# Performance work log

Hardware: AMD Instinct MI355X
Metric: run time of the kernel (lower is better)

Reference implementation:

```python
import jax, jax.numpy as jnp
import numpy as np

B, S, H = 2, 1024, 768
E, K, I = 16, 4, 768
ALPHA, LIMIT, EPS = 1.702, 7.0, 1e-5


def setup_inputs() -> dict:
    key = jax.random.key(0)
    ks = jax.random.split(key, 7)
    x = jax.random.normal(ks[0], (B, S, H), dtype=jnp.float32)
    scale = jnp.ones((H,), jnp.float32)                      # RMSNorm scale
    gate_w = jax.random.normal(ks[1], (E, H), jnp.float32) * 0.02
    gate_b = jnp.zeros((E,), jnp.float32)
    w1 = jax.random.normal(ks[2], (E, H, 2 * I), jnp.float32) * 0.02
    b1 = jax.random.normal(ks[3], (E, 2 * I), jnp.float32) * 0.02
    w2 = jax.random.normal(ks[4], (E, I, H), jnp.float32) * 0.02
    b2 = jax.random.normal(ks[5], (E, H), jnp.float32) * 0.02
    return {"x": x, "scale": scale, "gate_w": gate_w, "gate_b": gate_b,
            "w1": w1, "b1": b1, "w2": w2, "b2": b2}


def _swiglu(h):
    # chunk (not packed) split of last dim
    x_glu, x_lin = jnp.split(h, 2, axis=-1)
    x_glu = jnp.minimum(x_glu, LIMIT)
    x_lin = jnp.clip(x_lin, -LIMIT, LIMIT)
    return x_glu * jax.nn.sigmoid(ALPHA * x_glu) * (x_lin + 1.0)


def reference(x, scale, gate_w, gate_b, w1, b1, w2, b2):
    Bx, Sx, Hx = x.shape
    # RMSNorm in fp32 with learned scale
    xf = x.astype(jnp.float32)
    t = xf * jax.lax.rsqrt(jnp.mean(xf * xf, axis=-1, keepdims=True) + EPS) * scale
    t = t.reshape(-1, Hx)                                    # [T, H]
    T = t.shape[0]
    # Router: fp32 gate, top-k, softmax over selected logits, /K (re-scaled by K at combine)
    g = t @ gate_w.T + gate_b                                # [T, E]
    vals, idx = jax.lax.top_k(g, K)                          # [T, K]
    w = jax.nn.softmax(vals, axis=-1) / K                    # [T, K]
    # Scatter routing weights to dense [T, E]; unselected experts get weight 0,
    # so the dense per-expert compute below matches the gathered bmm path exactly.
    full_w = jnp.zeros((T, E), jnp.float32).at[jnp.arange(T)[:, None], idx].set(w)
    # Expert MLP1 + SwiGLU
    h = jnp.einsum('th,ehf->tef', t, w1) + b1                # [T, E, 2I]
    h = _swiglu(h)                                           # [T, E, I]
    # Expert MLP2
    y = jnp.einsum('tei,eih->teh', h, w2) + b2               # [T, E, H]
    # Weighted combine (einsum('bec,be->bc')) * experts_per_token
    out = jnp.einsum('teh,te->th', y, full_w) * K            # [T, H]
    # Residual connection
    return x + out.astype(x.dtype).reshape(Bx, Sx, Hx)
```

## Files before the change

### kernel.cpp

```cpp
#include <hip/hip_runtime.h>
#include <hip/hip_bf16.h>
#include <cstddef>

#define T_TOK 2048
#define H_DIM 768
#define NEXP 16
#define KSEL 4
#define I_DIM 768
#define TWO_I 1536
#define NSLOT (T_TOK*KSEL)
#define ALPHA 1.702f
#define LIMIT 7.0f
#define EPS_RMS 1e-5f
#define BM 128

typedef _Float16 f16;
typedef _Float16 half8 __attribute__((ext_vector_type(8)));
typedef float f32x4 __attribute__((ext_vector_type(4)));

__global__ __launch_bounds__(256) void k_rms_router(
    const float* __restrict__ x, const float* __restrict__ scale,
    const float* __restrict__ gw, const float* __restrict__ gb,
    f16* __restrict__ th, float* __restrict__ out,
    int* __restrict__ topk_idx, float* __restrict__ topk_w)
{
    int t = blockIdx.x;
    int tid = threadIdx.x;
    int lane = tid & 63, wid = tid >> 6;
    __shared__ float ts[H_DIM];
    __shared__ float red[8];
    __shared__ float logits[NEXP];

    const float* xr = x + (size_t)t * H_DIM;
    float v0 = xr[tid], v1 = xr[tid + 256], v2 = xr[tid + 512];
    float ss = v0*v0 + v1*v1 + v2*v2;
    #pragma unroll
    for (int m = 32; m >= 1; m >>= 1) ss += __shfl_xor(ss, m, 64);
    if (lane == 0) red[wid] = ss;
    __syncthreads();
    if (tid == 0) {
        float tot = red[0] + red[1] + red[2] + red[3];
        red[4] = rsqrtf(tot / (float)H_DIM + EPS_RMS);
    }
    __syncthreads();
    float rinv = red[4];
    float t0 = v0 * rinv * scale[tid];
    float t1 = v1 * rinv * scale[tid + 256];
    float t2 = v2 * rinv * scale[tid + 512];
    ts[tid] = t0; ts[tid + 256] = t1; ts[tid + 512] = t2;
    size_t base = (size_t)t * H_DIM;
    th[base + tid] = (f16)t0;
    th[base + tid + 256] = (f16)t1;
    th[base + tid + 512] = (f16)t2;
    float* op = out + base;
    op[tid] = v0; op[tid + 256] = v1; op[tid + 512] = v2;
    __syncthreads();

    #pragma unroll
    for (int ee = 0; ee < 4; ++ee) {
        int e = wid * 4 + ee;
        const float* g = gw + (size_t)e * H_DIM;
        float p = 0.f;
        for (int i = lane; i < H_DIM; i += 64) p += ts[i] * g[i];
        #pragma unroll
        for (int m = 32; m >= 1; m >>= 1) p += __shfl_xor(p, m, 64);
        if (lane == 0) logits[e] = p + gb[e];
    }
    __syncthreads();

    if (tid == 0) {
        float lg[NEXP];
        #pragma unroll
        for (int e = 0; e < NEXP; ++e) lg[e] = logits[e];
        float vals[KSEL]; int idx[KSEL];
        #pragma unroll
        for (int k = 0; k < KSEL; ++k) {
            float best = -1e30f; int bi = 0;
            for (int e = 0; e < NEXP; ++e)
                if (lg[e] > best) { best = lg[e]; bi = e; }
            vals[k] = best; idx[k] = bi; lg[bi] = -1e30f;
        }
        float mx = vals[0], sum = 0.f, ex[KSEL];
        #pragma unroll
        for (int k = 0; k < KSEL; ++k) { ex[k] = expf(vals[k] - mx); sum += ex[k]; }
        float inv = 1.f / sum;
        #pragma unroll
        for (int k = 0; k < KSEL; ++k) {
            topk_idx[t * KSEL + k] = idx[k];
            topk_w[t * KSEL + k] = ex[k] * inv;
        }
    }
}

__global__ __launch_bounds__(256) void k_count(
    const int* __restrict__ topk_idx, int* __restrict__ counts)
{
    int e = blockIdx.x;
    int tid = threadIdx.x;
    int c = 0;
    for (int i = tid; i < NSLOT; i += 256) c += (topk_idx[i] == e) ? 1 : 0;
    #pragma unroll
    for (int m = 32; m >= 1; m >>= 1) c += __shfl_xor(c, m, 64);
    __shared__ int r[4];
    if ((tid & 63) == 0) r[tid >> 6] = c;
    __syncthreads();
    if (tid == 0) counts[e] = r[0] + r[1] + r[2] + r[3];
}

__global__ void k_scan(const int* __restrict__ counts, int* __restrict__ offsets)
{
    if (threadIdx.x == 0) {
        int acc = 0;
        for (int e = 0; e < NEXP; ++e) { offsets[e] = acc; acc += counts[e]; }
        offsets[NEXP] = acc;
    }
}

__global__ __launch_bounds__(256) void k_place(
    const int* __restrict__ topk_idx, const float* __restrict__ topk_w,
    const int* __restrict__ offsets,
    int* __restrict__ expert_tokens, float* __restrict__ expert_wts)
{
    int e = blockIdx.x;
    int tid = threadIdx.x;
    __shared__ int ps[256];
    int base = tid * 32;
    int c = 0;
    #pragma unroll 8
    for (int j = 0; j < 32; ++j) c += (topk_idx[base + j] == e) ? 1 : 0;
    ps[tid] = c;
    __syncthreads();
    if (tid == 0) {
        int run = 0;
        for (int i = 0; i < 256; ++i) { int v = ps[i]; ps[i] = run; run += v; }
    }
    __syncthreads();
    int slot = offsets[e] + ps[tid];
    for (int j = 0; j < 32; ++j) {
        int i = base + j;
        if (topk_idx[i] == e) {
            expert_tokens[slot] = i >> 2;
            expert_wts[slot] = topk_w[i];
            ++slot;
        }
    }
}

__global__ __launch_bounds__(256) void k_gemm1(
    const f16* __restrict__ th, const float* __restrict__ w1,
    const float* __restrict__ b1,
    const int* __restrict__ expert_tokens, const int* __restrict__ offsets,
    f16* __restrict__ h_buf)
{
    int e = blockIdx.z;
    int beg = offsets[e];
    int cnt = offsets[e + 1] - beg;
    int m0 = blockIdx.y * BM;
    if (m0 >= cnt) return;
    int n0 = blockIdx.x * 64;
    int rows = min(BM, cnt - m0);

    __shared__ f16 A_h[BM][40];
    __shared__ f16 Bg_h[64][40];
    __shared__ f16 Bn_h[64][40];
    __shared__ int toks[BM];

    int tid = threadIdx.x;
    int w = tid >> 6, lane = tid & 63;
    if (tid < BM) toks[tid] = (tid < rows) ? expert_tokens[beg + m0 + tid] : -1;
    __syncthreads();

    int arow = tid >> 2, ach = tid & 3;
    int tokA0 = toks[arow], tokA1 = toks[arow + 64];
    int fr = lane & 15, fg = lane >> 4;
    int wr = w >> 1, wc = w & 1;

    const float* bgp = w1 + ((size_t)e * H_DIM + w * 8) * TWO_I + n0 + lane;

    half8 z8;
    #pragma unroll
    for (int j = 0; j < 8; ++j) z8[j] = (f16)0.f;

    f32x4 zero4 = {0.f, 0.f, 0.f, 0.f};
    f32x4 accg[4][2], accn[4][2];
    #pragma unroll
    for (int mi = 0; mi < 4; ++mi)
        #pragma unroll
        for (int s = 0; s < 2; ++s) { accg[mi][s] = zero4; accn[mi][s] = zero4; }

    half8 pah0, pah1;
    float pbg[8], pbn[8];

#define G1_PRELOAD(KK)                                                          \
    do {                                                                        \
        pah0 = (tokA0 >= 0) ? *(const half8*)(th + (size_t)tokA0 * H_DIM + (KK) + ach * 8) : z8; \
        pah1 = (tokA1 >= 0) ? *(const half8*)(th + (size_t)tokA1 * H_DIM + (KK) + ach * 8) : z8; \
        _Pragma("unroll")                                                       \
        for (int j = 0; j < 8; ++j) {                                           \
            pbg[j] = bgp[(size_t)((KK) + j) * TWO_I];                           \
            pbn[j] = bgp[(size_t)((KK) + j) * TWO_I + I_DIM];                   \
        }                                                                       \
    } while (0)

    G1_PRELOAD(0);

    for (int kk = 0; kk < H_DIM; kk += 32) {
        __syncthreads();
        *(half8*)&A_h[arow][ach * 8] = pah0;
        *(half8*)&A_h[arow + 64][ach * 8] = pah1;
        half8 vgh, vnh;
        #pragma unroll
        for (int j = 0; j < 8; ++j) {
            vgh[j] = (f16)pbg[j];
            vnh[j] = (f16)pbn[j];
        }
        *(half8*)&Bg_h[lane][w * 8] = vgh;
        *(half8*)&Bn_h[lane][w * 8] = vnh;
        __syncthreads();
        if (kk + 32 < H_DIM) G1_PRELOAD(kk + 32);

        half8 ah[4];
        #pragma unroll
        for (int mi = 0; mi < 4; ++mi)
            ah[mi] = *(const half8*)&A_h[wr * 64 + mi * 16 + fr][fg * 8];
        #pragma unroll
        for (int s = 0; s < 2; ++s) {
            int nb = wc * 32 + s * 16 + fr;
            half8 bgh = *(const half8*)&Bg_h[nb][fg * 8];
            half8 bnh = *(const half8*)&Bn_h[nb][fg * 8];
            #pragma unroll
            for (int mi = 0; mi < 4; ++mi) {
                accg[mi][s] = __builtin_amdgcn_mfma_f32_16x16x32_f16(ah[mi], bgh, accg[mi][s], 0, 0, 0);
                accn[mi][s] = __builtin_amdgcn_mfma_f32_16x16x32_f16(ah[mi], bnh, accn[mi][s], 0, 0, 0);
            }
        }
    }
#undef G1_PRELOAD

    const float* b1p = b1 + (size_t)e * TWO_I + n0;
    #pragma unroll
    for (int mi = 0; mi < 4; ++mi) {
        #pragma unroll
        for (int s = 0; s < 2; ++s) {
            #pragma unroll
            for (int r4 = 0; r4 < 4; ++r4) {
                int rt = wr * 64 + mi * 16 + fg * 4 + r4;
                if (rt >= rows) continue;
                int slot = beg + m0 + rt;
                int c = wc * 32 + s * 16 + fr;
                float hg = accg[mi][s][r4] + b1p[c];
                float hl2 = accn[mi][s][r4] + b1p[I_DIM + c];
                hg = fminf(hg, LIMIT);
                hl2 = fminf(fmaxf(hl2, -LIMIT), LIMIT);
                float sg = 1.f / (1.f + expf(-ALPHA * hg));
                h_buf[(size_t)slot * I_DIM + n0 + c] = (f16)(hg * sg * (hl2 + 1.f));
            }
        }
    }
}

__global__ __launch_bounds__(256) void k_gemm2(
    const f16* __restrict__ h_buf, const float* __restrict__ w2,
    const float* __restrict__ b2,
    const int* __restrict__ expert_tokens, const float* __restrict__ expert_wts,
    const int* __restrict__ offsets, float* __restrict__ out)
{
    int e = blockIdx.z;
    int beg = offsets[e];
    int cnt = offsets[e + 1] - beg;
    int m0 = blockIdx.y * BM;
    if (m0 >= cnt) return;
    int n0 = blockIdx.x * 64;
    int rows = min(BM, cnt - m0);

    __shared__ f16 A_h[BM][40];
    __shared__ f16 B_h[64][40];
    __shared__ int   toks[BM];
    __shared__ float wts[BM];

    int tid = threadIdx.x;
    int w = tid >> 6, lane = tid & 63;
    if (tid < BM) {
        bool ok = tid < rows;
        toks[tid] = ok ? expert_tokens[beg + m0 + tid] : -1;
        wts[tid]  = ok ? expert_wts[beg + m0 + tid] : 0.f;
    }
    __syncthreads();

    int arow = tid >> 2, ach = tid & 3;
    bool aok0 = arow < rows, aok1 = (arow + 64) < rows;
    int fr = lane & 15, fg = lane >> 4;
    int r0 = w * 32;

    const float* bp = w2 + ((size_t)e * I_DIM + w * 8) * H_DIM + n0 + lane;

    half8 z8;
    #pragma unroll
    for (int j = 0; j < 8; ++j) z8[j] = (f16)0.f;

    f32x4 zero4 = {0.f, 0.f, 0.f, 0.f};
    f32x4 acc[2][4];
    #pragma unroll
    for (int mi = 0; mi < 2; ++mi)
        #pragma unroll
        for (int s = 0; s < 4; ++s) acc[mi][s] = zero4;

    half8 pah0, pah1;
    float pb[8];

#define G2_PRELOAD(KK)                                                          \
    do {                                                                        \
        pah0 = aok0 ? *(const half8*)(h_buf + (size_t)(beg + m0 + arow) * I_DIM + (KK) + ach * 8) : z8; \
        pah1 = aok1 ? *(const half8*)(h_buf + (size_t)(beg + m0 + arow + 64) * I_DIM + (KK) + ach * 8) : z8; \
        _Pragma("unroll")                                                       \
        for (int j = 0; j < 8; ++j) pb[j] = bp[(size_t)((KK) + j) * H_DIM];     \
    } while (0)

    G2_PRELOAD(0);

    for (int kk = 0; kk < I_DIM; kk += 32) {
        __syncthreads();
        *(half8*)&A_h[arow][ach * 8] = pah0;
        *(half8*)&A_h[arow + 64][ach * 8] = pah1;
        half8 vbh;
        #pragma unroll
        for (int j = 0; j < 8; ++j) vbh[j] = (f16)pb[j];
        *(half8*)&B_h[lane][w * 8] = vbh;
        __syncthreads();
        if (kk + 32 < I_DIM) G2_PRELOAD(kk + 32);

        half8 ah[2];
        #pragma unroll
        for (int mi = 0; mi < 2; ++mi)
            ah[mi] = *(const half8*)&A_h[r0 + mi * 16 + fr][fg * 8];
        #pragma unroll
        for (int s = 0; s < 4; ++s) {
            half8 bh = *(const half8*)&B_h[s * 16 + fr][fg * 8];
            #pragma unroll
            for (int mi = 0; mi < 2; ++mi)
                acc[mi][s] = __builtin_amdgcn_mfma_f32_16x16x32_f16(ah[mi], bh, acc[mi][s], 0, 0, 0);
        }
    }
#undef G2_PRELOAD

    const float* b2p = b2 + (size_t)e * H_DIM + n0;
    #pragma unroll
    for (int mi = 0; mi < 2; ++mi) {
        #pragma unroll
        for (int s = 0; s < 4; ++s) {
            #pragma unroll
            for (int r4 = 0; r4 < 4; ++r4) {
                int rt = r0 + mi * 16 + fg * 4 + r4;
                if (rt >= rows) continue;
                int tok = toks[rt];
                float wgt = wts[rt];
                int c = s * 16 + fr;
                atomicAdd(out + (size_t)tok * H_DIM + n0 + c, wgt * (acc[mi][s][r4] + b2p[c]));
            }
        }
    }
}

extern "C" void kernel_launch(void* const* d_in, const int* in_sizes, int n_in,
                              void* d_out, int out_size, void* d_ws, size_t ws_size,
                              hipStream_t stream)
{
    const float* x     = (const float*)d_in[0];
    const float* scale = (const float*)d_in[1];
    const float* gw    = (const float*)d_in[2];
    const float* gb    = (const float*)d_in[3];
    const float* w1    = (const float*)d_in[4];
    const float* b1    = (const float*)d_in[5];
    const float* w2    = (const float*)d_in[6];
    const float* b2    = (const float*)d_in[7];
    float* out = (float*)d_out;

    char* ws = (char*)d_ws;
    f16* th    = (f16*)ws;                                 ws += (size_t)T_TOK * H_DIM * 2;
    f16* h_buf = (f16*)ws;                                 ws += (size_t)NSLOT * I_DIM * 2;
    float* topk_w        = (float*)ws;                     ws += NSLOT * 4;
    float* expert_wts    = (float*)ws;                     ws += NSLOT * 4;
    int*   topk_idx      = (int*)ws;                       ws += NSLOT * 4;
    int*   expert_tokens = (int*)ws;                       ws += NSLOT * 4;
    int*   counts        = (int*)ws;                       ws += NEXP * 4;
    int*   offsets       = (int*)ws;

    hipLaunchKernelGGL(k_rms_router, dim3(T_TOK), dim3(256), 0, stream,
                       x, scale, gw, gb, th, out, topk_idx, topk_w);
    hipLaunchKernelGGL(k_count, dim3(NEXP), dim3(256), 0, stream, topk_idx, counts);
    hipLaunchKernelGGL(k_scan, dim3(1), dim3(64), 0, stream, counts, offsets);
    hipLaunchKernelGGL(k_place, dim3(NEXP), dim3(256), 0, stream,
                       topk_idx, topk_w, offsets, expert_tokens, expert_wts);
    hipLaunchKernelGGL(k_gemm1, dim3(I_DIM / 64, T_TOK / BM, NEXP), dim3(256), 0, stream,
                       th, w1, b1, expert_tokens, offsets, h_buf);
    hipLaunchKernelGGL(k_gemm2, dim3(H_DIM / 64, T_TOK / BM, NEXP), dim3(256), 0, stream,
                       h_buf, w2, b2, expert_tokens, expert_wts, offsets, out);
}
```

Before: 306.1 us.

## Merge routing kernels, double-buffer register prefetch, remap block order in expert GEMMs

Replaces the count, scan and place kernels with one single-block routing kernel that uses shared-memory atomics, removing two launches. Both expert GEMMs now keep two register prefetch stages so global loads run two k-steps ahead, and they carry a launch-bounds occupancy hint. Block indices are remapped so that neighbouring blocks in launch order come from different experts and tiles, spreading weight reads. Slot order within each expert is no longer deterministic, and the extra prefetch registers may lower occupancy.

```diff
diff --git a/kernel.cpp b/kernel.cpp
--- a/kernel.cpp
+++ b/kernel.cpp
@@ -92,72 +92,53 @@
     }
 }
 
-__global__ __launch_bounds__(256) void k_count(
-    const int* __restrict__ topk_idx, int* __restrict__ counts)
-{
-    int e = blockIdx.x;
-    int tid = threadIdx.x;
-    int c = 0;
-    for (int i = tid; i < NSLOT; i += 256) c += (topk_idx[i] == e) ? 1 : 0;
-    #pragma unroll
-    for (int m = 32; m >= 1; m >>= 1) c += __shfl_xor(c, m, 64);
-    __shared__ int r[4];
-    if ((tid & 63) == 0) r[tid >> 6] = c;
-    __syncthreads();
-    if (tid == 0) counts[e] = r[0] + r[1] + r[2] + r[3];
-}
-
-__global__ void k_scan(const int* __restrict__ counts, int* __restrict__ offsets)
-{
-    if (threadIdx.x == 0) {
-        int acc = 0;
-        for (int e = 0; e < NEXP; ++e) { offsets[e] = acc; acc += counts[e]; }
-        offsets[NEXP] = acc;
-    }
-}
-
-__global__ __launch_bounds__(256) void k_place(
+__global__ __launch_bounds__(256) void k_route(
     const int* __restrict__ topk_idx, const float* __restrict__ topk_w,
-    const int* __restrict__ offsets,
+    int* __restrict__ offsets,
     int* __restrict__ expert_tokens, float* __restrict__ expert_wts)
 {
-    int e = blockIdx.x;
+    __shared__ int cnt[NEXP];
+    __shared__ int cur[NEXP];
     int tid = threadIdx.x;
-    __shared__ int ps[256];
+    if (tid < NEXP) cnt[tid] = 0;
+    __syncthreads();
     int base = tid * 32;
-    int c = 0;
-    #pragma unroll 8
-    for (int j = 0; j < 32; ++j) c += (topk_idx[base + j] == e) ? 1 : 0;
-    ps[tid] = c;
+    for (int j = 0; j < 32; ++j) atomicAdd(&cnt[topk_idx[base + j]], 1);
     __syncthreads();
     if (tid == 0) {
-        int run = 0;
-        for (int i = 0; i < 256; ++i) { int v = ps[i]; ps[i] = run; run += v; }
-    }
-    __syncthreads();
-    int slot = offsets[e] + ps[tid];
+        int acc = 0;
+        for (int e = 0; e < NEXP; ++e) {
+            offsets[e] = acc; cur[e] = acc; acc += cnt[e];
+        }
+        offsets[NEXP] = acc;
+    }
+    __syncthreads();
     for (int j = 0; j < 32; ++j) {
         int i = base + j;
-        if (topk_idx[i] == e) {
-            expert_tokens[slot] = i >> 2;
-            expert_wts[slot] = topk_w[i];
-            ++slot;
-        }
+        int e = topk_idx[i];
+        int slot = atomicAdd(&cur[e], 1);
+        expert_tokens[slot] = i >> 2;
+        expert_wts[slot] = topk_w[i];
     }
 }
 
-__global__ __launch_bounds__(256) void k_gemm1(
+__global__ __launch_bounds__(256, 4) void k_gemm1(
     const f16* __restrict__ th, const float* __restrict__ w1,
     const float* __restrict__ b1,
     const int* __restrict__ expert_tokens, const int* __restrict__ offsets,
     f16* __restrict__ h_buf)
 {
-    int e = blockIdx.z;
+    int lid = blockIdx.x + 12 * (blockIdx.y + 16 * blockIdx.z);
+    int tl = (lid & 7) * 384 + (lid >> 3);
+    int by = tl & 15;
+    int bx = (tl >> 4) % 12;
+    int e  = tl / 192;
+
     int beg = offsets[e];
     int cnt = offsets[e + 1] - beg;
-    int m0 = blockIdx.y * BM;
+    int m0 = by * BM;
     if (m0 >= cnt) return;
-    int n0 = blockIdx.x * 64;
+    int n0 = bx * 64;
     int rows = min(BM, cnt - m0);
 
     __shared__ f16 A_h[BM][40];
@@ -188,54 +169,69 @@
         #pragma unroll
         for (int s = 0; s < 2; ++s) { accg[mi][s] = zero4; accn[mi][s] = zero4; }
 
-    half8 pah0, pah1;
-    float pbg[8], pbn[8];
-
-#define G1_PRELOAD(KK)                                                          \
-    do {                                                                        \
-        pah0 = (tokA0 >= 0) ? *(const half8*)(th + (size_t)tokA0 * H_DIM + (KK) + ach * 8) : z8; \
-        pah1 = (tokA1 >= 0) ? *(const half8*)(th + (size_t)tokA1 * H_DIM + (KK) + ach * 8) : z8; \
+    half8 pah0A, pah1A, pah0B, pah1B;
+    float pbgA[8], pbnA[8], pbgB[8], pbnB[8];
+
+#define G1_PRELOAD(S, KK)                                                       \
+    {                                                                           \
+        pah0##S = (tokA0 >= 0) ? *(const half8*)(th + (size_t)tokA0 * H_DIM + (KK) + ach * 8) : z8; \
+        pah1##S = (tokA1 >= 0) ? *(const half8*)(th + (size_t)tokA1 * H_DIM + (KK) + ach * 8) : z8; \
         _Pragma("unroll")                                                       \
         for (int j = 0; j < 8; ++j) {                                           \
-            pbg[j] = bgp[(size_t)((KK) + j) * TWO_I];                           \
-            pbn[j] = bgp[(size_t)((KK) + j) * TWO_I + I_DIM];                   \
+            pbg##S[j] = bgp[(size_t)((KK) + j) * TWO_I];                        \
+            pbn##S[j] = bgp[(size_t)((KK) + j) * TWO_I + I_DIM];                \
         }                                                                       \
-    } while (0)
-
-    G1_PRELOAD(0);
-
-    for (int kk = 0; kk < H_DIM; kk += 32) {
-        __syncthreads();
-        *(half8*)&A_h[arow][ach * 8] = pah0;
-        *(half8*)&A_h[arow + 64][ach * 8] = pah1;
-        half8 vgh, vnh;
-        #pragma unroll
-        for (int j = 0; j < 8; ++j) {
-            vgh[j] = (f16)pbg[j];
-            vnh[j] = (f16)pbn[j];
-        }
-        *(half8*)&Bg_h[lane][w * 8] = vgh;
-        *(half8*)&Bn_h[lane][w * 8] = vnh;
-        __syncthreads();
-        if (kk + 32 < H_DIM) G1_PRELOAD(kk + 32);
-
-        half8 ah[4];
-        #pragma unroll
-        for (int mi = 0; mi < 4; ++mi)
-            ah[mi] = *(const half8*)&A_h[wr * 64 + mi * 16 + fr][fg * 8];
-        #pragma unroll
-        for (int s = 0; s < 2; ++s) {
-            int nb = wc * 32 + s * 16 + fr;
-            half8 bgh = *(const half8*)&Bg_h[nb][fg * 8];
-            half8 bnh = *(const half8*)&Bn_h[nb][fg * 8];
-            #pragma unroll
-            for (int mi = 0; mi < 4; ++mi) {
-                accg[mi][s] = __builtin_amdgcn_mfma_f32_16x16x32_f16(ah[mi], bgh, accg[mi][s], 0, 0, 0);
-                accn[mi][s] = __builtin_amdgcn_mfma_f32_16x16x32_f16(ah[mi], bnh, accn[mi][s], 0, 0, 0);
-            }
-        }
+    }
+
+#define G1_STAGE(S)                                                             \
+    {                                                                           \
+        *(half8*)&A_h[arow][ach * 8] = pah0##S;                                 \
+        *(half8*)&A_h[arow + 64][ach * 8] = pah1##S;                            \
+        half8 vg, vn;                                                           \
+        _Pragma("unroll")                                                       \
+        for (int j = 0; j < 8; ++j) { vg[j] = (f16)pbg##S[j]; vn[j] = (f16)pbn##S[j]; } \
+        *(half8*)&Bg_h[lane][w * 8] = vg;                                       \
+        *(half8*)&Bn_h[lane][w * 8] = vn;                                       \
+    }
+
+#define G1_COMPUTE()                                                            \
+    {                                                                           \
+        half8 ah[4];                                                            \
+        _Pragma("unroll")                                                       \
+        for (int mi = 0; mi < 4; ++mi)                                          \
+            ah[mi] = *(const half8*)&A_h[wr * 64 + mi * 16 + fr][fg * 8];       \
+        _Pragma("unroll")                                                       \
+        for (int s = 0; s < 2; ++s) {                                           \
+            int nb = wc * 32 + s * 16 + fr;                                     \
+            half8 bgh = *(const half8*)&Bg_h[nb][fg * 8];                       \
+            half8 bnh = *(const half8*)&Bn_h[nb][fg * 8];                       \
+            _Pragma("unroll")                                                   \
+            for (int mi = 0; mi < 4; ++mi) {                                    \
+                accg[mi][s] = __builtin_amdgcn_mfma_f32_16x16x32_f16(ah[mi], bgh, accg[mi][s], 0, 0, 0); \
+                accn[mi][s] = __builtin_amdgcn_mfma_f32_16x16x32_f16(ah[mi], bnh, accn[mi][s], 0, 0, 0); \
+            }                                                                   \
+        }                                                                       \
+    }
+
+    G1_PRELOAD(A, 0);
+    G1_STAGE(A);
+    __syncthreads();
+    G1_PRELOAD(B, 32);
+
+    for (int kk = 0; kk < H_DIM; kk += 64) {
+        if (kk + 64 < H_DIM) G1_PRELOAD(A, kk + 64);
+        G1_COMPUTE();
+        __syncthreads();
+        G1_STAGE(B);
+        __syncthreads();
+        if (kk + 96 < H_DIM) G1_PRELOAD(B, kk + 96);
+        G1_COMPUTE();
+        __syncthreads();
+        if (kk + 64 < H_DIM) { G1_STAGE(A); __syncthreads(); }
     }
 #undef G1_PRELOAD
+#undef G1_STAGE
+#undef G1_COMPUTE
 
     const float* b1p = b1 + (size_t)e * TWO_I + n0;
     #pragma unroll
@@ -259,18 +255,23 @@
     }
 }
 
-__global__ __launch_bounds__(256) void k_gemm2(
+__global__ __launch_bounds__(256, 4) void k_gemm2(
     const f16* __restrict__ h_buf, const float* __restrict__ w2,
     const float* __restrict__ b2,
     const int* __restrict__ expert_tokens, const float* __restrict__ expert_wts,
     const int* __restrict__ offsets, float* __restrict__ out)
 {
-    int e = blockIdx.z;
+    int lid = blockIdx.x + 12 * (blockIdx.y + 16 * blockIdx.z);
+    int tl = (lid & 7) * 384 + (lid >> 3);
+    int by = tl & 15;
+    int bx = (tl >> 4) % 12;
+    int e  = tl / 192;
+
     int beg = offsets[e];
     int cnt = offsets[e + 1] - beg;
-    int m0 = blockIdx.y * BM;
+    int m0 = by * BM;
     if (m0 >= cnt) return;
-    int n0 = blockIdx.x * 64;
+    int n0 = bx * 64;
     int rows = min(BM, cnt - m0);
 
     __shared__ f16 A_h[BM][40];
@@ -305,43 +306,61 @@
         #pragma unroll
         for (int s = 0; s < 4; ++s) acc[mi][s] = zero4;
 
-    half8 pah0, pah1;
-    float pb[8];
-
-#define G2_PRELOAD(KK)                                                          \
-    do {                                                                        \
-        pah0 = aok0 ? *(const half8*)(h_buf + (size_t)(beg + m0 + arow) * I_DIM + (KK) + ach * 8) : z8; \
-        pah1 = aok1 ? *(const half8*)(h_buf + (size_t)(beg + m0 + arow + 64) * I_DIM + (KK) + ach * 8) : z8; \
-        _Pragma("unroll")                                                       \
-        for (int j = 0; j < 8; ++j) pb[j] = bp[(size_t)((KK) + j) * H_DIM];     \
-    } while (0)
-
-    G2_PRELOAD(0);
-
-    for (int kk = 0; kk < I_DIM; kk += 32) {
-        __syncthreads();
-        *(half8*)&A_h[arow][ach * 8] = pah0;
-        *(half8*)&A_h[arow + 64][ach * 8] = pah1;
-        half8 vbh;
-        #pragma unroll
-        for (int j = 0; j < 8; ++j) vbh[j] = (f16)pb[j];
-        *(half8*)&B_h[lane][w * 8] = vbh;
-        __syncthreads();
-        if (kk + 32 < I_DIM) G2_PRELOAD(kk + 32);
-
-        half8 ah[2];
-        #pragma unroll
-        for (int mi = 0; mi < 2; ++mi)
-            ah[mi] = *(const half8*)&A_h[r0 + mi * 16 + fr][fg * 8];
-        #pragma unroll
-        for (int s = 0; s < 4; ++s) {
-            half8 bh = *(const half8*)&B_h[s * 16 + fr][fg * 8];
-            #pragma unroll
-            for (int mi = 0; mi < 2; ++mi)
-                acc[mi][s] = __builtin_amdgcn_mfma_f32_16x16x32_f16(ah[mi], bh, acc[mi][s], 0, 0, 0);
-        }
+    half8 pah0A, pah1A, pah0B, pah1B;
+    float pbA[8], pbB[8];
+
+#define G2_PRELOAD(S, KK)                                                       \
+    {                                                                           \
+        pah0##S = aok0 ? *(const half8*)(h_buf + (size_t)(beg + m0 + arow) * I_DIM + (KK) + ach * 8) : z8; \
+        pah1##S = aok1 ? *(const half8*)(h_buf + (size_t)(beg + m0 + arow + 64) * I_DIM + (KK) + ach * 8) : z8; \
+        _Pragma("unroll")                                                       \
+        for (int j = 0; j < 8; ++j) pb##S[j] = bp[(size_t)((KK) + j) * H_DIM];  \
+    }
+
+#define G2_STAGE(S)                                                             \
+    {                                                                           \
+        *(half8*)&A_h[arow][ach * 8] = pah0##S;                                 \
+        *(half8*)&A_h[arow + 64][ach * 8] = pah1##S;                            \
+        half8 vb;                                                               \
+        _Pragma("unroll")                                                       \
+        for (int j = 0; j < 8; ++j) vb[j] = (f16)pb##S[j];                      \
+        *(half8*)&B_h[lane][w * 8] = vb;                                        \
+    }
+
+#define G2_COMPUTE()                                                            \
+    {                                                                           \
+        half8 ah[2];                                                            \
+        _Pragma("unroll")                                                       \
+        for (int mi = 0; mi < 2; ++mi)                                          \
+            ah[mi] = *(const half8*)&A_h[r0 + mi * 16 + fr][fg * 8];            \
+        _Pragma("unroll")                                                       \
+        for (int s = 0; s < 4; ++s) {                                           \
+            half8 bh = *(const half8*)&B_h[s * 16 + fr][fg * 8];                \
+            _Pragma("unroll")                                                   \
+            for (int mi = 0; mi < 2; ++mi)                                      \
+                acc[mi][s] = __builtin_amdgcn_mfma_f32_16x16x32_f16(ah[mi], bh, acc[mi][s], 0, 0, 0); \
+        }                                                                       \
+    }
+
+    G2_PRELOAD(A, 0);
+    G2_STAGE(A);
+    __syncthreads();
+    G2_PRELOAD(B, 32);
+
+    for (int kk = 0; kk < I_DIM; kk += 64) {
+        if (kk + 64 < I_DIM) G2_PRELOAD(A, kk + 64);
+        G2_COMPUTE();
+        __syncthreads();
+        G2_STAGE(B);
+        __syncthreads();
+        if (kk + 96 < I_DIM) G2_PRELOAD(B, kk + 96);
+        G2_COMPUTE();
+        __syncthreads();
+        if (kk + 64 < I_DIM) { G2_STAGE(A); __syncthreads(); }
     }
 #undef G2_PRELOAD
+#undef G2_STAGE
+#undef G2_COMPUTE
 
     const float* b2p = b2 + (size_t)e * H_DIM + n0;
     #pragma unroll
@@ -382,14 +401,11 @@
     float* expert_wts    = (float*)ws;                     ws += NSLOT * 4;
     int*   topk_idx      = (int*)ws;                       ws += NSLOT * 4;
     int*   expert_tokens = (int*)ws;                       ws += NSLOT * 4;
-    int*   counts        = (int*)ws;                       ws += NEXP * 4;
     int*   offsets       = (int*)ws;
 
     hipLaunchKernelGGL(k_rms_router, dim3(T_TOK), dim3(256), 0, stream,
                        x, scale, gw, gb, th, out, topk_idx, topk_w);
-    hipLaunchKernelGGL(k_count, dim3(NEXP), dim3(256), 0, stream, topk_idx, counts);
-    hipLaunchKernelGGL(k_scan, dim3(1), dim3(64), 0, stream, counts, offsets);
-    hipLaunchKernelGGL(k_place, dim3(NEXP), dim3(256), 0, stream,
+    hipLaunchKernelGGL(k_route, dim3(1), dim3(256), 0, stream,
                        topk_idx, topk_w, offsets, expert_tokens, expert_wts);
     hipLaunchKernelGGL(k_gemm1, dim3(I_DIM / 64, T_TOK / BM, NEXP), dim3(256), 0, stream,
                        th, w1, b1, expert_tokens, offsets, h_buf);
```

Result: slower. 528.7 us (+72.7%).

## Fuse routing kernels into one atomic pass and remap GEMM block order

Applied to the files above, without the earlier changes.

Replaces the count, scan and place kernels with a single one-block kernel that counts experts with shared-memory atomics, scans, and scatters slots with atomics. This removes two launches and the redundant per-expert passes over topk_idx. The GEMM kernels also remap the linear block id so that consecutive blocks are spread across 8 groups, presumably to balance work across XCDs and improve cache locality. Atomic placement makes slot order within an expert nondeterministic, which changes accumulation order only for each token's own row.

```diff
diff --git a/kernel.cpp b/kernel.cpp
--- a/kernel.cpp
+++ b/kernel.cpp
@@ -92,57 +92,33 @@
     }
 }
 
-__global__ __launch_bounds__(256) void k_count(
-    const int* __restrict__ topk_idx, int* __restrict__ counts)
-{
-    int e = blockIdx.x;
+__global__ __launch_bounds__(256) void k_route(
+    const int* __restrict__ topk_idx, const float* __restrict__ topk_w,
+    int* __restrict__ offsets,
+    int* __restrict__ expert_tokens, float* __restrict__ expert_wts)
+{
+    __shared__ int cnt[NEXP];
+    __shared__ int cur[NEXP];
     int tid = threadIdx.x;
-    int c = 0;
-    for (int i = tid; i < NSLOT; i += 256) c += (topk_idx[i] == e) ? 1 : 0;
-    #pragma unroll
-    for (int m = 32; m >= 1; m >>= 1) c += __shfl_xor(c, m, 64);
-    __shared__ int r[4];
-    if ((tid & 63) == 0) r[tid >> 6] = c;
-    __syncthreads();
-    if (tid == 0) counts[e] = r[0] + r[1] + r[2] + r[3];
-}
-
-__global__ void k_scan(const int* __restrict__ counts, int* __restrict__ offsets)
-{
-    if (threadIdx.x == 0) {
+    if (tid < NEXP) cnt[tid] = 0;
+    __syncthreads();
+    int base = tid * 32;
+    for (int j = 0; j < 32; ++j) atomicAdd(&cnt[topk_idx[base + j]], 1);
+    __syncthreads();
+    if (tid == 0) {
         int acc = 0;
-        for (int e = 0; e < NEXP; ++e) { offsets[e] = acc; acc += counts[e]; }
+        for (int e = 0; e < NEXP; ++e) {
+            offsets[e] = acc; cur[e] = acc; acc += cnt[e];
+        }
         offsets[NEXP] = acc;
     }
-}
-
-__global__ __launch_bounds__(256) void k_place(
-    const int* __restrict__ topk_idx, const float* __restrict__ topk_w,
-    const int* __restrict__ offsets,
-    int* __restrict__ expert_tokens, float* __restrict__ expert_wts)
-{
-    int e = blockIdx.x;
-    int tid = threadIdx.x;
-    __shared__ int ps[256];
-    int base = tid * 32;
-    int c = 0;
-    #pragma unroll 8
-    for (int j = 0; j < 32; ++j) c += (topk_idx[base + j] == e) ? 1 : 0;
-    ps[tid] = c;
-    __syncthreads();
-    if (tid == 0) {
-        int run = 0;
-        for (int i = 0; i < 256; ++i) { int v = ps[i]; ps[i] = run; run += v; }
-    }
-    __syncthreads();
-    int slot = offsets[e] + ps[tid];
+    __syncthreads();
     for (int j = 0; j < 32; ++j) {
         int i = base + j;
-        if (topk_idx[i] == e) {
-            expert_tokens[slot] = i >> 2;
-            expert_wts[slot] = topk_w[i];
-            ++slot;
-        }
+        int e = topk_idx[i];
+        int slot = atomicAdd(&cur[e], 1);
+        expert_tokens[slot] = i >> 2;
+        expert_wts[slot] = topk_w[i];
     }
 }
 
@@ -152,12 +128,17 @@
     const int* __restrict__ expert_tokens, const int* __restrict__ offsets,
     f16* __restrict__ h_buf)
 {
-    int e = blockIdx.z;
+    int lid = blockIdx.x + 12 * (blockIdx.y + 16 * blockIdx.z);
+    int tl = (lid & 7) * 384 + (lid >> 3);
+    int by = tl & 15;
+    int bx = (tl >> 4) % 12;
+    int e  = tl / 192;
+
     int beg = offsets[e];
     int cnt = offsets[e + 1] - beg;
-    int m0 = blockIdx.y * BM;
+    int m0 = by * BM;
     if (m0 >= cnt) return;
-    int n0 = blockIdx.x * 64;
+    int n0 = bx * 64;
     int rows = min(BM, cnt - m0);
 
     __shared__ f16 A_h[BM][40];
@@ -265,12 +246,17 @@
     const int* __restrict__ expert_tokens, const float* __restrict__ expert_wts,
     const int* __restrict__ offsets, float* __restrict__ out)
 {
-    int e = blockIdx.z;
+    int lid = blockIdx.x + 12 * (blockIdx.y + 16 * blockIdx.z);
+    int tl = (lid & 7) * 384 + (lid >> 3);
+    int by = tl & 15;
+    int bx = (tl >> 4) % 12;
+    int e  = tl / 192;
+
     int beg = offsets[e];
     int cnt = offsets[e + 1] - beg;
-    int m0 = blockIdx.y * BM;
+    int m0 = by * BM;
     if (m0 >= cnt) return;
-    int n0 = blockIdx.x * 64;
+    int n0 = bx * 64;
     int rows = min(BM, cnt - m0);
 
     __shared__ f16 A_h[BM][40];
@@ -382,14 +368,11 @@
     float* expert_wts    = (float*)ws;                     ws += NSLOT * 4;
     int*   topk_idx      = (int*)ws;                       ws += NSLOT * 4;
     int*   expert_tokens = (int*)ws;                       ws += NSLOT * 4;
-    int*   counts        = (int*)ws;                       ws += NEXP * 4;
     int*   offsets       = (int*)ws;
 
     hipLaunchKernelGGL(k_rms_router, dim3(T_TOK), dim3(256), 0, stream,
                        x, scale, gw, gb, th, out, topk_idx, topk_w);
-    hipLaunchKernelGGL(k_count, dim3(NEXP), dim3(256), 0, stream, topk_idx, counts);
-    hipLaunchKernelGGL(k_scan, dim3(1), dim3(64), 0, stream, counts, offsets);
-    hipLaunchKernelGGL(k_place, dim3(NEXP), dim3(256), 0, stream,
+    hipLaunchKernelGGL(k_route, dim3(1), dim3(256), 0, stream,
                        topk_idx, topk_w, offsets, expert_tokens, expert_wts);
     hipLaunchKernelGGL(k_gemm1, dim3(I_DIM / 64, T_TOK / BM, NEXP), dim3(256), 0, stream,
                        th, w1, b1, expert_tokens, offsets, h_buf);
```

Result: slower. 336.3 us (+9.9%).
